# Optimization experiments

Measured on AMD Instinct MI355X. Metric: run time of the kernel, lower is better.

Reference implementation:

```python
import jax, jax.numpy as jnp
import numpy as np

E, IN, OUT, T = 8, 4096, 4096, 8192
GS = IN  # groupsize=-1 -> groupsize = infeatures


def setup_inputs() -> dict:
    key = jax.random.key(0)
    k1, k2, k3, k4, k5 = jax.random.split(key, 5)
    x = jax.random.normal(k1, (T, IN), dtype=jnp.float16)
    indices = jax.random.randint(k2, (T,), 0, E, dtype=jnp.int32)
    # int32 words each packing 8 int4 nonzero values (2:4 sparse -> IN*OUT/2 values per expert)
    qweight = jax.random.randint(k3, (E, IN // 32, OUT * 16 // 8), 0, 2**31 - 1, dtype=jnp.int32)
    meta = jax.random.randint(k4, (E, OUT, IN // 16), 0, 2**15, dtype=jnp.int32).astype(jnp.int16)
    scales = (jax.random.uniform(k5, (E, IN // GS, OUT), dtype=jnp.float32) * 0.02 + 0.001).astype(jnp.float16)
    return {"x": x, "indices": indices, "qweight": qweight, "meta": meta, "scales": scales}


def _dequant_24(qweight, meta, scales):
    """Decode packed int4 + 2:4-sparsity metadata into dense fp32 weights (E, OUT, IN)."""
    # unpack 8 int4 nibbles per int32 word, symmetric zero-point 8
    nib = (qweight[..., None] >> (4 * jnp.arange(8, dtype=jnp.int32))) & 0xF  # (E, IN//32, 2*OUT, 8)
    vals = nib.reshape(E, IN // 2, OUT).transpose(0, 2, 1).astype(jnp.float32) - 8.0  # (E, OUT, IN//2)
    m = meta.astype(jnp.int32) & 0xFFFF
    sub = (m[..., None] >> (2 * jnp.arange(8, dtype=jnp.int32))) & 0x3  # (E, OUT, IN//16, 8)
    grp = (jnp.arange(8, dtype=jnp.int32) // 2) * 4                      # group-of-4 base within 16-block
    base = 16 * jnp.arange(IN // 16, dtype=jnp.int32)                    # 16-block base
    dense_col = (base[None, None, :, None] + grp[None, None, None, :] + sub).reshape(E, OUT, IN // 2)
    eidx = jnp.arange(E)[:, None, None]
    oidx = jnp.arange(OUT)[None, :, None]
    W = jnp.zeros((E, OUT, IN), jnp.float32).at[eidx, oidx, dense_col].add(vals)
    # per-group dequant scales: (E, IN//GS, OUT) -> (E, OUT, IN)
    s = jnp.repeat(scales.astype(jnp.float32), GS, axis=1).transpose(0, 2, 1)
    return W * s


def reference(x, indices, qweight, meta, scales):
    W = _dequant_24(qweight, meta, scales)  # (E, OUT, IN)
    y = jnp.zeros((x.shape[0], OUT), jnp.float32)
    for e in range(E):  # fixed small expert count
        xe = jnp.where((indices == e)[:, None], x, 0).astype(jnp.float32)
        y = y + xe @ W[e].T
    return y.astype(x.dtype)
```

## Files before the change

### kernel.cpp

```cpp
#include <hip/hip_runtime.h>

#define E_N   8
#define IN_N  4096
#define OUT_N 4096
#define T_N   8192

#define BM 128
#define BN 256
#define BK 64
#define LDK (BK + 8)
#define NTHREADS 512

typedef unsigned short u16;
typedef __bf16 bf16_t;
typedef bf16_t bf16x8 __attribute__((ext_vector_type(8)));
typedef u16    u16x8  __attribute__((ext_vector_type(8)));
typedef float  f32x4  __attribute__((ext_vector_type(4)));

__device__ int g_cnt[E_N];
__device__ int g_base[E_N];
__device__ int g_ids[T_N];
__device__ int g_meta_wide;
__device__ u16 g_W[(long)E_N * OUT_N * IN_N];
__device__ u16 g_xb[(long)T_N * IN_N];

__device__ __forceinline__ u16 f2bf(float f) {
    unsigned u = __builtin_bit_cast(unsigned, f);
    u += 0x7FFFu + ((u >> 16) & 1u);
    return (u16)(u >> 16);
}

__global__ void sort_tokens(const int* __restrict__ idx, const u16* __restrict__ meta16) {
    __shared__ int cnt[E_N], off[E_N];
    __shared__ int probe;
    const int tid = threadIdx.x;
    if (tid == 0) probe = 0;
    if (tid < E_N) cnt[tid] = 0;
    __syncthreads();
    if (tid < 64) {
        unsigned v = meta16[2 * (tid * 131072) + 1];
        if (v) atomicOr(&probe, 1);
    }
    for (int t = tid; t < T_N; t += blockDim.x) atomicAdd(&cnt[idx[t] & 7], 1);
    __syncthreads();
    if (tid == 0) {
        int s = 0;
        for (int e = 0; e < E_N; ++e) { g_cnt[e] = cnt[e]; g_base[e] = s; off[e] = s; s += cnt[e]; }
        g_meta_wide = (probe == 0) ? 1 : 0;
    }
    __syncthreads();
    for (int t = tid; t < T_N; t += blockDim.x) {
        int p = atomicAdd(&off[idx[t] & 7], 1);
        if (p >= 0 && p < T_N) g_ids[p] = t;
    }
}

__global__ __launch_bounds__(256, 4)
void xb_convert(const float* __restrict__ x) {
    const int p = blockIdx.x;
    int tok = g_ids[p];
    if ((unsigned)tok >= (unsigned)T_N) tok = 0;
    const float* src = x + (long)tok * IN_N;
    u16* dst = g_xb + (long)p * IN_N;
    const int tid = threadIdx.x;
    float va[16];
    #pragma unroll
    for (int c4 = 0; c4 < 4; ++c4) {
        float4 v = *reinterpret_cast<const float4*>(src + tid * 16 + c4 * 4);
        va[c4 * 4 + 0] = v.x; va[c4 * 4 + 1] = v.y; va[c4 * 4 + 2] = v.z; va[c4 * 4 + 3] = v.w;
    }
    unsigned wp[8];
    #pragma unroll
    for (int p8 = 0; p8 < 8; ++p8)
        wp[p8] = (unsigned)f2bf(va[2 * p8]) | ((unsigned)f2bf(va[2 * p8 + 1]) << 16);
    *reinterpret_cast<int4*>(dst + tid * 16)     = make_int4((int)wp[0], (int)wp[1], (int)wp[2], (int)wp[3]);
    *reinterpret_cast<int4*>(dst + tid * 16 + 8) = make_int4((int)wp[4], (int)wp[5], (int)wp[6], (int)wp[7]);
}

__global__ __launch_bounds__(NTHREADS, 1)
void decode_w(const int* __restrict__ qw, const void* __restrict__ meta) {
    const int e  = blockIdx.z;
    const int n0 = blockIdx.x * BN;
    const int kt = blockIdx.y;
    const bool mwide = (g_meta_wide != 0);
    const int tid = threadIdx.x;
    #pragma unroll
    for (int it = 0; it < 2; ++it) {
        const int idx2 = tid + it * NTHREADS;
        const int c  = idx2 & (BN - 1);
        const int gi = idx2 >> 8;
        const int o  = n0 + c;
        const int g  = kt * 4 + gi;
        const int midx = (e * OUT_N + o) * (IN_N / 16) + g;
        unsigned mw;
        if (mwide) mw = (unsigned)((const int*)meta)[midx] & 0xFFFFu;
        else       mw = (unsigned)((const u16*)meta)[midx];
        const unsigned sh = (o & 7) << 2;
        const int* qp = qw + ((e * (IN_N / 32) + (g >> 1)) << 13) + (o >> 3) + ((g & 1) << 12);
        int d[16];
        #pragma unroll
        for (int p = 0; p < 16; ++p) d[p] = 0;
        #pragma unroll
        for (int grp = 0; grp < 4; ++grp) {
            const unsigned w0 = (unsigned)qp[(2 * grp) * 512];
            const unsigned w1 = (unsigned)qp[(2 * grp + 1) * 512];
            const int v0 = (int)((w0 >> sh) & 0xF) - 8;
            const int v1 = (int)((w1 >> sh) & 0xF) - 8;
            const int s0 = (mw >> (4 * grp)) & 3;
            const int s1 = (mw >> (4 * grp + 2)) & 3;
            #pragma unroll
            for (int q = 0; q < 4; ++q) {
                int t0 = (s0 == q) ? v0 : 0;
                int t1 = (s1 == q) ? v1 : 0;
                d[grp * 4 + q] = t0 + t1;
            }
        }
        unsigned wp[8];
        #pragma unroll
        for (int p = 0; p < 8; ++p) {
            unsigned lo = __builtin_bit_cast(unsigned, (float)d[2 * p])     >> 16;
            unsigned hi = __builtin_bit_cast(unsigned, (float)d[2 * p + 1]) >> 16;
            wp[p] = lo | (hi << 16);
        }
        u16* wr = g_W + ((long)e * OUT_N + o) * IN_N + kt * 64 + gi * 16;
        *reinterpret_cast<int4*>(wr)     = make_int4((int)wp[0], (int)wp[1], (int)wp[2], (int)wp[3]);
        *reinterpret_cast<int4*>(wr + 8) = make_int4((int)wp[4], (int)wp[5], (int)wp[6], (int)wp[7]);
    }
}

__global__ __launch_bounds__(NTHREADS, 1)
void moe_gemm(const float* __restrict__ scales, float* __restrict__ y) {
    const int e = blockIdx.z;
    int cnt = g_cnt[e];
    if (cnt < 0) cnt = 0;
    if (cnt > T_N) cnt = T_N;
    const int m0 = blockIdx.y * BM;
    if (m0 >= cnt) return;
    const int n0 = blockIdx.x * BN;
    int base = g_base[e];
    if (base < 0) base = 0;
    if (base > T_N - cnt) base = T_N - cnt;

    __shared__ __align__(16) u16 As[BM][LDK];
    __shared__ __align__(16) u16 Bs[BN][LDK];

    const int tid  = threadIdx.x;
    const int lane = tid & 63;
    const int wid  = tid >> 6;
    const int wm   = wid >> 2;
    const int wn   = wid & 3;

    const int ar = tid >> 2;
    const int aq = tid & 3;
    long arow = (long)base + m0 + ar;
    if (arow > T_N - 1) arow = T_N - 1;
    const u16* axp = g_xb + arow * IN_N;
    const int br = tid >> 1;
    const int bh = tid & 1;
    const u16* bxp = g_W + ((long)e * OUT_N + n0 + br) * IN_N;

    f32x4 acc[4][4];
    #pragma unroll
    for (int i = 0; i < 4; ++i)
        #pragma unroll
        for (int j = 0; j < 4; ++j) acc[i][j] = (f32x4){0.f, 0.f, 0.f, 0.f};

    for (int k0 = 0; k0 < IN_N; k0 += BK) {
        int4 a0 = *reinterpret_cast<const int4*>(axp + k0 + aq * 16);
        int4 a1 = *reinterpret_cast<const int4*>(axp + k0 + aq * 16 + 8);
        int4 b0 = *reinterpret_cast<const int4*>(bxp + k0 + bh * 32);
        int4 b1 = *reinterpret_cast<const int4*>(bxp + k0 + bh * 32 + 8);
        int4 b2 = *reinterpret_cast<const int4*>(bxp + k0 + bh * 32 + 16);
        int4 b3 = *reinterpret_cast<const int4*>(bxp + k0 + bh * 32 + 24);
        *reinterpret_cast<int4*>(&As[ar][aq * 16])      = a0;
        *reinterpret_cast<int4*>(&As[ar][aq * 16 + 8])  = a1;
        *reinterpret_cast<int4*>(&Bs[br][bh * 32])      = b0;
        *reinterpret_cast<int4*>(&Bs[br][bh * 32 + 8])  = b1;
        *reinterpret_cast<int4*>(&Bs[br][bh * 32 + 16]) = b2;
        *reinterpret_cast<int4*>(&Bs[br][bh * 32 + 24]) = b3;
        __syncthreads();
        #pragma unroll
        for (int kk = 0; kk < BK; kk += 32) {
            bf16x8 af[4], bfr[4];
            #pragma unroll
            for (int mf = 0; mf < 4; ++mf) {
                u16x8 r = *reinterpret_cast<const u16x8*>(&As[wm * 64 + mf * 16 + (lane & 15)][kk + ((lane >> 4) << 3)]);
                af[mf] = __builtin_bit_cast(bf16x8, r);
            }
            #pragma unroll
            for (int nf = 0; nf < 4; ++nf) {
                u16x8 r = *reinterpret_cast<const u16x8*>(&Bs[wn * 64 + nf * 16 + (lane & 15)][kk + ((lane >> 4) << 3)]);
                bfr[nf] = __builtin_bit_cast(bf16x8, r);
            }
            #pragma unroll
            for (int mf = 0; mf < 4; ++mf)
                #pragma unroll
                for (int nf = 0; nf < 4; ++nf)
                    acc[mf][nf] = __builtin_amdgcn_mfma_f32_16x16x32_bf16(af[mf], bfr[nf], acc[mf][nf], 0, 0, 0);
        }
        __syncthreads();
    }

    const int* toks = g_ids + base;
    float sc[4];
    #pragma unroll
    for (int nf = 0; nf < 4; ++nf)
        sc[nf] = scales[e * OUT_N + n0 + wn * 64 + nf * 16 + (lane & 15)];
    #pragma unroll
    for (int mf = 0; mf < 4; ++mf) {
        #pragma unroll
        for (int r = 0; r < 4; ++r) {
            const int row = m0 + wm * 64 + mf * 16 + ((lane >> 4) << 2) + r;
            if (row >= cnt) continue;
            int tok = toks[row];
            if ((unsigned)tok >= (unsigned)T_N) continue;
            float* yrow = y + (long)tok * OUT_N;
            #pragma unroll
            for (int nf = 0; nf < 4; ++nf) {
                const int col = n0 + wn * 64 + nf * 16 + (lane & 15);
                yrow[col] = acc[mf][nf][r] * sc[nf];
            }
        }
    }
}

extern "C" void kernel_launch(void* const* d_in, const int* in_sizes, int n_in,
                              void* d_out, int out_size, void* d_ws, size_t ws_size,
                              hipStream_t stream) {
    const float* x      = nullptr;
    const int* indices  = nullptr;
    const int* qw       = nullptr;
    const void* meta    = nullptr;
    const float* scales = nullptr;
    int big_seen = 0;
    for (int i = 0; i < n_in; ++i) {
        long s = in_sizes[i];
        if (s == 33554432L)      x = (const float*)d_in[i];
        else if (s == 8192L)     indices = (const int*)d_in[i];
        else if (s == 32768L)    scales = (const float*)d_in[i];
        else if (s == 8388608L) {
            if (big_seen++ == 0)  qw = (const int*)d_in[i];
            else                  meta = d_in[i];
        }
    }
    if (!x || !indices || !qw || !meta || !scales) return;
    float* y = (float*)d_out;

    hipLaunchKernelGGL(sort_tokens, dim3(1), dim3(1024), 0, stream, indices, (const u16*)meta);
    hipLaunchKernelGGL(xb_convert, dim3(T_N), dim3(256), 0, stream, x);
    hipLaunchKernelGGL(decode_w, dim3(OUT_N / BN, IN_N / BK, E_N), dim3(NTHREADS), 0, stream, qw, meta);
    hipLaunchKernelGGL(moe_gemm, dim3(OUT_N / BN, T_N / BM, E_N), dim3(NTHREADS), 0, stream, scales, y);
}
```

Measured before the change: 630.6 us.

## Tile-major decoded weights and async global-to-LDS loads in GEMM

The decode kernel now writes dense weights in a k-tile-major layout (e, kt, OUT, 64), so each GEMM tile of B is one contiguous block. Each decode thread handles one output row across four k-tiles and loads its metadata up front. The GEMM uses global_load_lds to copy A and B straight into unpadded LDS, skipping the register round trip. Removing the padding risks LDS bank conflicts on the MFMA fragment reads, and there is still no double-buffering.

```diff
diff --git a/kernel.cpp b/kernel.cpp
--- a/kernel.cpp
+++ b/kernel.cpp
@@ -8,7 +8,6 @@
 #define BM 128
 #define BN 256
 #define BK 64
-#define LDK (BK + 8)
 #define NTHREADS 512
 
 typedef unsigned short u16;
@@ -16,6 +15,11 @@
 typedef bf16_t bf16x8 __attribute__((ext_vector_type(8)));
 typedef u16    u16x8  __attribute__((ext_vector_type(8)));
 typedef float  f32x4  __attribute__((ext_vector_type(4)));
+
+#define GLOAD16(gsrc, ldst) \
+    __builtin_amdgcn_global_load_lds( \
+        (const __attribute__((address_space(1))) unsigned int*)(gsrc), \
+        (__attribute__((address_space(3))) unsigned int*)(ldst), 16, 0, 0)
 
 __device__ int g_cnt[E_N];
 __device__ int g_base[E_N];
@@ -77,54 +81,62 @@
     *reinterpret_cast<int4*>(dst + tid * 16 + 8) = make_int4((int)wp[4], (int)wp[5], (int)wp[6], (int)wp[7]);
 }
 
-__global__ __launch_bounds__(NTHREADS, 1)
+__global__ __launch_bounds__(256, 4)
 void decode_w(const int* __restrict__ qw, const void* __restrict__ meta) {
-    const int e  = blockIdx.z;
-    const int n0 = blockIdx.x * BN;
-    const int kt = blockIdx.y;
+    const int e   = blockIdx.z;
+    const int kt0 = blockIdx.y * 4;
+    const int o   = blockIdx.x * 256 + threadIdx.x;
     const bool mwide = (g_meta_wide != 0);
-    const int tid = threadIdx.x;
-    #pragma unroll
-    for (int it = 0; it < 2; ++it) {
-        const int idx2 = tid + it * NTHREADS;
-        const int c  = idx2 & (BN - 1);
-        const int gi = idx2 >> 8;
-        const int o  = n0 + c;
-        const int g  = kt * 4 + gi;
-        const int midx = (e * OUT_N + o) * (IN_N / 16) + g;
-        unsigned mw;
-        if (mwide) mw = (unsigned)((const int*)meta)[midx] & 0xFFFFu;
-        else       mw = (unsigned)((const u16*)meta)[midx];
-        const unsigned sh = (o & 7) << 2;
-        const int* qp = qw + ((e * (IN_N / 32) + (g >> 1)) << 13) + (o >> 3) + ((g & 1) << 12);
-        int d[16];
-        #pragma unroll
-        for (int p = 0; p < 16; ++p) d[p] = 0;
-        #pragma unroll
-        for (int grp = 0; grp < 4; ++grp) {
-            const unsigned w0 = (unsigned)qp[(2 * grp) * 512];
-            const unsigned w1 = (unsigned)qp[(2 * grp + 1) * 512];
-            const int v0 = (int)((w0 >> sh) & 0xF) - 8;
-            const int v1 = (int)((w1 >> sh) & 0xF) - 8;
-            const int s0 = (mw >> (4 * grp)) & 3;
-            const int s1 = (mw >> (4 * grp + 2)) & 3;
-            #pragma unroll
-            for (int q = 0; q < 4; ++q) {
-                int t0 = (s0 == q) ? v0 : 0;
-                int t1 = (s1 == q) ? v1 : 0;
-                d[grp * 4 + q] = t0 + t1;
-            }
-        }
-        unsigned wp[8];
-        #pragma unroll
-        for (int p = 0; p < 8; ++p) {
-            unsigned lo = __builtin_bit_cast(unsigned, (float)d[2 * p])     >> 16;
-            unsigned hi = __builtin_bit_cast(unsigned, (float)d[2 * p + 1]) >> 16;
-            wp[p] = lo | (hi << 16);
-        }
-        u16* wr = g_W + ((long)e * OUT_N + o) * IN_N + kt * 64 + gi * 16;
-        *reinterpret_cast<int4*>(wr)     = make_int4((int)wp[0], (int)wp[1], (int)wp[2], (int)wp[3]);
-        *reinterpret_cast<int4*>(wr + 8) = make_int4((int)wp[4], (int)wp[5], (int)wp[6], (int)wp[7]);
+    unsigned mws[16];
+    if (mwide) {
+        const int* mp = (const int*)meta + ((long)e * OUT_N + o) * (IN_N / 16) + kt0 * 4;
+        #pragma unroll
+        for (int i = 0; i < 16; ++i) mws[i] = (unsigned)mp[i] & 0xFFFFu;
+    } else {
+        const u16* mp = (const u16*)meta + ((long)e * OUT_N + o) * (IN_N / 16) + kt0 * 4;
+        #pragma unroll
+        for (int i = 0; i < 16; ++i) mws[i] = mp[i];
+    }
+    const unsigned sh = (o & 7) << 2;
+    #pragma unroll
+    for (int ki = 0; ki < 4; ++ki) {
+        const int kt = kt0 + ki;
+        unsigned wp[32];
+        #pragma unroll
+        for (int gi = 0; gi < 4; ++gi) {
+            const int g = kt * 4 + gi;
+            const unsigned mw = mws[ki * 4 + gi];
+            const int* qp = qw + ((e * (IN_N / 32) + (g >> 1)) << 13) + (o >> 3) + ((g & 1) << 12);
+            int d[16];
+            #pragma unroll
+            for (int p = 0; p < 16; ++p) d[p] = 0;
+            #pragma unroll
+            for (int grp = 0; grp < 4; ++grp) {
+                const unsigned w0 = (unsigned)qp[(2 * grp) * 512];
+                const unsigned w1 = (unsigned)qp[(2 * grp + 1) * 512];
+                const int v0 = (int)((w0 >> sh) & 0xF) - 8;
+                const int v1 = (int)((w1 >> sh) & 0xF) - 8;
+                const int s0 = (mw >> (4 * grp)) & 3;
+                const int s1 = (mw >> (4 * grp + 2)) & 3;
+                #pragma unroll
+                for (int q = 0; q < 4; ++q) {
+                    int t0 = (s0 == q) ? v0 : 0;
+                    int t1 = (s1 == q) ? v1 : 0;
+                    d[grp * 4 + q] = t0 + t1;
+                }
+            }
+            #pragma unroll
+            for (int p = 0; p < 8; ++p) {
+                unsigned lo = __builtin_bit_cast(unsigned, (float)d[2 * p])     >> 16;
+                unsigned hi = __builtin_bit_cast(unsigned, (float)d[2 * p + 1]) >> 16;
+                wp[gi * 8 + p] = lo | (hi << 16);
+            }
+        }
+        u16* wr = g_W + ((long)(e * 64 + kt) * OUT_N + o) * 64;
+        #pragma unroll
+        for (int q4 = 0; q4 < 8; ++q4)
+            *reinterpret_cast<int4*>(wr + q4 * 8) =
+                make_int4((int)wp[q4 * 4], (int)wp[q4 * 4 + 1], (int)wp[q4 * 4 + 2], (int)wp[q4 * 4 + 3]);
     }
 }
 
@@ -141,23 +153,22 @@
     if (base < 0) base = 0;
     if (base > T_N - cnt) base = T_N - cnt;
 
-    __shared__ __align__(16) u16 As[BM][LDK];
-    __shared__ __align__(16) u16 Bs[BN][LDK];
+    __shared__ __align__(16) u16 As[BM * BK];
+    __shared__ __align__(16) u16 Bs[BN * BK];
 
     const int tid  = threadIdx.x;
     const int lane = tid & 63;
-    const int wid  = tid >> 6;
-    const int wm   = wid >> 2;
-    const int wn   = wid & 3;
-
-    const int ar = tid >> 2;
-    const int aq = tid & 3;
-    long arow = (long)base + m0 + ar;
-    if (arow > T_N - 1) arow = T_N - 1;
-    const u16* axp = g_xb + arow * IN_N;
-    const int br = tid >> 1;
-    const int bh = tid & 1;
-    const u16* bxp = g_W + ((long)e * OUT_N + n0 + br) * IN_N;
+    const int wm   = (tid >> 6) >> 2;
+    const int wn   = (tid >> 6) & 3;
+
+    const int r0 = tid >> 3, kc = tid & 7;
+    long ar0 = (long)base + m0 + r0;       if (ar0 > T_N - 1) ar0 = T_N - 1;
+    long ar1 = (long)base + m0 + 64 + r0;  if (ar1 > T_N - 1) ar1 = T_N - 1;
+    const u16* asrc0 = g_xb + ar0 * IN_N + kc * 8;
+    const u16* asrc1 = g_xb + ar1 * IN_N + kc * 8;
+    u16* adst0 = &As[tid * 8];
+    u16* adst1 = &As[(tid + 512) * 8];
+    const u16* bsrc = g_W + ((long)e * 64 * OUT_N + n0) * 64 + tid * 8;
 
     f32x4 acc[4][4];
     #pragma unroll
@@ -166,31 +177,27 @@
         for (int j = 0; j < 4; ++j) acc[i][j] = (f32x4){0.f, 0.f, 0.f, 0.f};
 
     for (int k0 = 0; k0 < IN_N; k0 += BK) {
-        int4 a0 = *reinterpret_cast<const int4*>(axp + k0 + aq * 16);
-        int4 a1 = *reinterpret_cast<const int4*>(axp + k0 + aq * 16 + 8);
-        int4 b0 = *reinterpret_cast<const int4*>(bxp + k0 + bh * 32);
-        int4 b1 = *reinterpret_cast<const int4*>(bxp + k0 + bh * 32 + 8);
-        int4 b2 = *reinterpret_cast<const int4*>(bxp + k0 + bh * 32 + 16);
-        int4 b3 = *reinterpret_cast<const int4*>(bxp + k0 + bh * 32 + 24);
-        *reinterpret_cast<int4*>(&As[ar][aq * 16])      = a0;
-        *reinterpret_cast<int4*>(&As[ar][aq * 16 + 8])  = a1;
-        *reinterpret_cast<int4*>(&Bs[br][bh * 32])      = b0;
-        *reinterpret_cast<int4*>(&Bs[br][bh * 32 + 8])  = b1;
-        *reinterpret_cast<int4*>(&Bs[br][bh * 32 + 16]) = b2;
-        *reinterpret_cast<int4*>(&Bs[br][bh * 32 + 24]) = b3;
+        GLOAD16(asrc0 + k0, adst0);
+        GLOAD16(asrc1 + k0, adst1);
+        #pragma unroll
+        for (int it = 0; it < 4; ++it)
+            GLOAD16(bsrc + it * 4096, &Bs[(tid + it * 512) * 8]);
+        bsrc += (long)OUT_N * 64;
         __syncthreads();
         #pragma unroll
         for (int kk = 0; kk < BK; kk += 32) {
             bf16x8 af[4], bfr[4];
             #pragma unroll
             for (int mf = 0; mf < 4; ++mf) {
-                u16x8 r = *reinterpret_cast<const u16x8*>(&As[wm * 64 + mf * 16 + (lane & 15)][kk + ((lane >> 4) << 3)]);
-                af[mf] = __builtin_bit_cast(bf16x8, r);
+                const int r = wm * 64 + mf * 16 + (lane & 15);
+                u16x8 v = *reinterpret_cast<const u16x8*>(&As[r * 64 + kk + ((lane >> 4) << 3)]);
+                af[mf] = __builtin_bit_cast(bf16x8, v);
             }
             #pragma unroll
             for (int nf = 0; nf < 4; ++nf) {
-                u16x8 r = *reinterpret_cast<const u16x8*>(&Bs[wn * 64 + nf * 16 + (lane & 15)][kk + ((lane >> 4) << 3)]);
-                bfr[nf] = __builtin_bit_cast(bf16x8, r);
+                const int r = wn * 64 + nf * 16 + (lane & 15);
+                u16x8 v = *reinterpret_cast<const u16x8*>(&Bs[r * 64 + kk + ((lane >> 4) << 3)]);
+                bfr[nf] = __builtin_bit_cast(bf16x8, v);
             }
             #pragma unroll
             for (int mf = 0; mf < 4; ++mf)
@@ -248,6 +255,6 @@
 
     hipLaunchKernelGGL(sort_tokens, dim3(1), dim3(1024), 0, stream, indices, (const u16*)meta);
     hipLaunchKernelGGL(xb_convert, dim3(T_N), dim3(256), 0, stream, x);
-    hipLaunchKernelGGL(decode_w, dim3(OUT_N / BN, IN_N / BK, E_N), dim3(NTHREADS), 0, stream, qw, meta);
+    hipLaunchKernelGGL(decode_w, dim3(OUT_N / 256, 16, E_N), dim3(256), 0, stream, qw, meta);
     hipLaunchKernelGGL(moe_gemm, dim3(OUT_N / BN, T_N / BM, E_N), dim3(NTHREADS), 0, stream, scales, y);
 }
```

Result: slower. 725.5 us (+15.1%).
